# Optimization experiments

Hardware: AMD Instinct MI355X
Metric: run time of the kernel (lower is better)

Reference implementation:

```python
import jax, jax.numpy as jnp
import numpy as np

B, S, H = 2, 2048, 3072
NH, NKV, HD = 24, 8, 128  # num_heads, num_kv_heads, head_dim


def setup_inputs() -> dict:
    key = jax.random.key(0)
    ks = jax.random.split(key, 5)
    scale = 0.02
    return {
        "hidden_states": jax.random.normal(ks[0], (B, S, H), dtype=jnp.float32),
        "attention_mask": jnp.zeros((B, 1, S, S), dtype=jnp.float32),
        "Wq": jax.random.normal(ks[1], (H, NH * HD), dtype=jnp.float32) * scale,
        "Wk": jax.random.normal(ks[2], (H, NKV * HD), dtype=jnp.float32) * scale,
        "Wv": jax.random.normal(ks[3], (H, NKV * HD), dtype=jnp.float32) * scale,
        "Wo": jax.random.normal(ks[4], (NH * HD, H), dtype=jnp.float32) * scale,
    }


def reference(hidden_states, attention_mask, Wq, Wk, Wv, Wo):
    b, s, _ = hidden_states.shape
    n_rep = NH // NKV
    # projections
    q = (hidden_states @ Wq).reshape(b, s, NH, HD).transpose(0, 2, 1, 3)   # [B,NH,S,D]
    k = (hidden_states @ Wk).reshape(b, s, NKV, HD).transpose(0, 2, 1, 3)  # [B,NKV,S,D]
    v = (hidden_states @ Wv).reshape(b, s, NKV, HD).transpose(0, 2, 1, 3)
    # grouped-query attention: view q as [B, NKV, n_rep, S, D]; avoids materializing repeated KV
    qg = q.reshape(b, NKV, n_rep, s, HD)
    scores = jnp.einsum("bgrqd,bgkd->bgrqk", qg, k) / jnp.sqrt(jnp.float32(HD))
    scores = scores.reshape(b, NH, s, s) + attention_mask
    attn = jax.nn.softmax(scores.astype(jnp.float32), axis=-1).astype(q.dtype)
    out = jnp.einsum("bgrqk,bgkd->bgrqd", attn.reshape(b, NKV, n_rep, s, s), v)
    out = out.reshape(b, NH, s, HD).transpose(0, 2, 1, 3).reshape(b, s, NH * HD)
    return out @ Wo
```

## Files before the change

### kernel.cpp

```cpp
#include <hip/hip_runtime.h>
#include <hip/hip_bf16.h>
#include <stdint.h>

typedef __attribute__((ext_vector_type(8))) short short8;
typedef __attribute__((ext_vector_type(4))) float f32x4;
typedef __attribute__((ext_vector_type(16))) float f32x16;

#define DEVINL static __device__ __forceinline__

DEVINL unsigned short f2bf(float x) {
  union { float f; unsigned int u; } c; c.f = x;
  unsigned int u = c.u;
  u += 0x7fffu + ((u >> 16) & 1u);
  return (unsigned short)(u >> 16);
}

DEVINL float bf2f(unsigned short x) {
  union { unsigned int u; float f; } c; c.u = ((unsigned int)x) << 16;
  return c.f;
}

DEVINL f32x4 mfma16(short8 a, short8 b, f32x4 c) {
  return __builtin_amdgcn_mfma_f32_16x16x32_bf16(a, b, c, 0, 0, 0);
}

DEVINL f32x16 mfma32(short8 a, short8 b, f32x16 c) {
  return __builtin_amdgcn_mfma_f32_32x32x16_bf16(a, b, c, 0, 0, 0);
}

DEVINL unsigned int cvtpk(float lo, float hi_) {
  unsigned int r;
  asm("v_cvt_pk_bf16_f32 %0, %1, %2" : "=v"(r) : "v"(lo), "v"(hi_));
  return r;
}

DEVINL void pl32swap(unsigned int& a, unsigned int& b) {
  asm("v_permlane32_swap_b32 %0, %1" : "+v"(a), "+v"(b));
}

DEVINL void gload16(const void* g, void* l) {
  __builtin_amdgcn_global_load_lds((const __attribute__((address_space(1))) void*)g,
                                   (__attribute__((address_space(3))) void*)l, 16, 0, 0);
}

static constexpr int BB = 2, SS = 2048, HH = 3072;
static constexpr int NH = 24, NKV = 8, HD = 128, NREP = 3;
static constexpr int MM = BB * SS;
static constexpr int KQ = NH * HD;
static constexpr int KKV = NKV * HD;

__global__ void k_cvt(const float* __restrict__ in, unsigned short* __restrict__ out,
                      int n, float scale) {
  int i = (blockIdx.x * 256 + threadIdx.x) * 4;
  if (i >= n) return;
  float4 v = *reinterpret_cast<const float4*>(in + i);
  ushort4 o;
  o.x = f2bf(v.x * scale); o.y = f2bf(v.y * scale);
  o.z = f2bf(v.z * scale); o.w = f2bf(v.w * scale);
  *reinterpret_cast<ushort4*>(out + i) = o;
}

__global__ void k_tcvt(const float* __restrict__ in, unsigned short* __restrict__ out,
                       int R, int C) {
  __shared__ float t[32][33];
  int tx = threadIdx.x & 31, ty = threadIdx.x >> 5;
  int r0 = blockIdx.y * 32, c0 = blockIdx.x * 32;
#pragma unroll
  for (int i = 0; i < 32; i += 8)
    t[ty + i][tx] = in[(long)(r0 + ty + i) * C + c0 + tx];
  __syncthreads();
#pragma unroll
  for (int i = 0; i < 32; i += 8)
    out[(long)(c0 + ty + i) * R + r0 + tx] = f2bf(t[tx][ty + i]);
}

__global__ void k_vt(const unsigned short* __restrict__ V, unsigned short* __restrict__ VT) {
  __shared__ unsigned short t[32][33];
  int b = blockIdx.z >> 3, kv = blockIdx.z & 7;
  int tx = threadIdx.x & 31, ty = threadIdx.x >> 5;
  int d0 = blockIdx.x * 32, s0 = blockIdx.y * 32;
  const unsigned short* src = V + ((long)b * SS) * KKV + kv * HD;
  unsigned short* dst = VT + (long)(b * NKV + kv) * HD * SS;
#pragma unroll
  for (int i = 0; i < 32; i += 8)
    t[ty + i][tx] = src[(long)(s0 + ty + i) * KKV + d0 + tx];
  __syncthreads();
#pragma unroll
  for (int i = 0; i < 32; i += 8)
    dst[(long)(d0 + ty + i) * SS + s0 + tx] = t[tx][ty + i];
}

template <typename OutT>
__global__ __launch_bounds__(256, 2) void k_gemm(const unsigned short* __restrict__ A,
                                                 const unsigned short* __restrict__ Bt,
                                                 OutT* __restrict__ C,
                                                 int M, int N, int K) {
  __shared__ alignas(16) unsigned short As[128 * 64];
  __shared__ alignas(16) unsigned short Bs[128 * 64];
  const int tid = threadIdx.x;
  const int wave = tid >> 6, lane = tid & 63;
  const int l15 = lane & 15, g = lane >> 4;
  const int wr = wave >> 1, wc = wave & 1;
  const long m0 = (long)blockIdx.y * 128, n0 = (long)blockIdx.x * 128;

  f32x4 acc[4][4] = {{{0.f,0.f,0.f,0.f}}};

  for (long k0 = 0; k0 < K; k0 += 64) {
#pragma unroll
    for (int j = 0; j < 4; ++j) {
      int idx = j * 256 + wave * 64 + lane;
      int row = idx >> 3, sub = idx & 7;
      int sc_ = (sub ^ (row & 7)) * 8;
      gload16(A  + (m0 + row) * K + k0 + sc_, (char*)As + (j * 4 + wave) * 1024);
      gload16(Bt + (n0 + row) * K + k0 + sc_, (char*)Bs + (j * 4 + wave) * 1024);
    }
    __syncthreads();
#pragma unroll
    for (int ks = 0; ks < 2; ++ks) {
      short8 a[4], b[4];
#pragma unroll
      for (int m = 0; m < 4; ++m) {
        int row = wr * 64 + m * 16 + l15;
        int cb = (ks * 64 + g * 16) ^ ((row & 7) << 4);
        a[m] = *reinterpret_cast<const short8*>((const char*)As + row * 128 + cb);
      }
#pragma unroll
      for (int n = 0; n < 4; ++n) {
        int row = wc * 64 + n * 16 + l15;
        int cb = (ks * 64 + g * 16) ^ ((row & 7) << 4);
        b[n] = *reinterpret_cast<const short8*>((const char*)Bs + row * 128 + cb);
      }
#pragma unroll
      for (int m = 0; m < 4; ++m)
#pragma unroll
        for (int n = 0; n < 4; ++n)
          acc[m][n] = mfma16(a[m], b[n], acc[m][n]);
    }
    __syncthreads();
  }

#pragma unroll
  for (int m = 0; m < 4; ++m)
#pragma unroll
    for (int n = 0; n < 4; ++n)
#pragma unroll
      for (int r = 0; r < 4; ++r) {
        long row = m0 + wr * 64 + m * 16 + g * 4 + r;
        long col = n0 + wc * 64 + n * 16 + l15;
        float v = acc[m][n][r];
        if constexpr (sizeof(OutT) == 2) C[row * N + col] = f2bf(v);
        else                             C[row * N + col] = v;
      }
}

__global__ __launch_bounds__(256, 3) void k_attn(const unsigned short* __restrict__ Q,
                                                 const unsigned short* __restrict__ Kb,
                                                 const unsigned short* __restrict__ VT,
                                                 const unsigned short* __restrict__ Mb,
                                                 unsigned short* __restrict__ AO) {
  const int tid = threadIdx.x;
  const int wave = tid >> 6, lane = tid & 63;
  const int l31 = lane & 31, hi = lane >> 5;

  const int bid = blockIdx.x;
  const int id = (bid & 7) * 96 + (bid >> 3);
  const int qt = id & 15;
  const int h  = (id >> 4) % NH;
  const int b  = id / (16 * NH);
  const int kv = h / NREP;
  const int qb = qt * 128 + wave * 32;

  const unsigned short* Qp = Q + ((long)b * SS + qb) * KQ + h * HD;
  const unsigned short* Kp = Kb + (long)b * SS * KKV + kv * HD;
  const unsigned short* Vp = VT + (long)(b * NKV + kv) * HD * SS;
  const unsigned short* Mp = Mb + (long)b * SS * SS + (long)(qb + l31) * SS;

  __shared__ alignas(16) unsigned short Ks[2][64 * 128];
  __shared__ alignas(16) unsigned short Vs[128 * 64];

  const float SC2 = 0.08838834764831845f * 1.4426950408889634f;

  short8 qf[8];
#pragma unroll
  for (int c = 0; c < 8; ++c)
    qf[c] = *reinterpret_cast<const short8*>(Qp + (long)l31 * KQ + c * 16 + hi * 8);

  f32x16 o[4];
#pragma unroll
  for (int dc = 0; dc < 4; ++dc)
#pragma unroll
    for (int r = 0; r < 16; ++r) o[dc][r] = 0.f;
  float mrun = -3e38f, lrun = 0.f;

  auto stageK = [&](int buf, int kt) {
#pragma unroll
    for (int j = 0; j < 4; ++j) {
      int idx = j * 256 + wave * 64 + lane;
      int row = idx >> 4, s = idx & 15;
      int ss = (s & 8) | ((s ^ row) & 7);
      gload16(Kp + (long)(kt + row) * KKV + ss * 8,
              (char*)Ks[buf] + (j * 4 + wave) * 1024);
    }
  };
  auto stageV = [&](int kt) {
#pragma unroll
    for (int j = 0; j < 4; ++j) {
      int idx = j * 256 + wave * 64 + lane;
      int row = idx >> 3, s = idx & 7;
      int ss = s ^ (row & 7);
      gload16(Vp + (long)row * SS + kt + ss * 8,
              (char*)Vs + (j * 4 + wave) * 1024);
    }
  };

  stageK(0, 0);
  __syncthreads();

  for (int t = 0; t < SS / 64; ++t) {
    const int kt = t * 64;
    stageV(kt);
    if (t < SS / 64 - 1) stageK((t + 1) & 1, kt + 64);
    const char* Kt = (const char*)Ks[t & 1];

    f32x16 sc0, sc1;
#pragma unroll
    for (int r = 0; r < 16; ++r) { sc0[r] = 0.f; sc1[r] = 0.f; }
    __builtin_amdgcn_s_setprio(1);
#pragma unroll
    for (int sb = 0; sb < 2; ++sb) {
      const int row = sb * 32 + l31;
#pragma unroll
      for (int ch = 0; ch < 2; ++ch) {
        short8 kf[4];
#pragma unroll
        for (int cc = 0; cc < 4; ++cc) {
          int c = ch * 4 + cc;
          int s = c * 2 + hi;
          int ss = (s & 8) | ((s ^ (row & 7)) & 7);
          kf[cc] = *reinterpret_cast<const short8*>(Kt + row * 256 + ss * 16);
        }
#pragma unroll
        for (int cc = 0; cc < 4; ++cc) {
          if (sb == 0) sc0 = mfma32(kf[cc], qf[ch * 4 + cc], sc0);
          else         sc1 = mfma32(kf[cc], qf[ch * 4 + cc], sc1);
        }
      }
    }
    __builtin_amdgcn_s_setprio(0);

    float tm = -3e38f;
#pragma unroll
    for (int sb = 0; sb < 2; ++sb) {
#pragma unroll
      for (int u = 0; u < 4; ++u) {
        ushort4 mk = *reinterpret_cast<const ushort4*>(Mp + kt + sb * 32 + u * 8 + hi * 4);
#pragma unroll
        for (int e = 0; e < 4; ++e) {
          int r = u * 4 + e;
          float x = (sb ? sc1[r] : sc0[r]) * SC2 + bf2f((&mk.x)[e]);
          if (sb) sc1[r] = x; else sc0[r] = x;
          tm = fmaxf(tm, x);
        }
      }
    }
    tm = fmaxf(tm, __shfl_xor(tm, 32));

    if (!__all(tm <= mrun + 8.f)) {
      float mn = fmaxf(mrun, tm);
      float corr = __builtin_amdgcn_exp2f(mrun - mn);
      mrun = mn;
      lrun *= corr;
#pragma unroll
      for (int r = 0; r < 16; ++r) {
        int qrow = (r & 3) + 8 * (r >> 2) + 4 * hi;
        float cr = __shfl(corr, qrow);
#pragma unroll
        for (int dc = 0; dc < 4; ++dc) o[dc][r] *= cr;
      }
    }

    float ts = 0.f;
#pragma unroll
    for (int r = 0; r < 16; ++r) {
      float p0 = __builtin_amdgcn_exp2f(sc0[r] - mrun);
      float p1 = __builtin_amdgcn_exp2f(sc1[r] - mrun);
      sc0[r] = p0; sc1[r] = p1;
      ts += p0 + p1;
    }
    ts += __shfl_xor(ts, 32);
    lrun += ts;

    __syncthreads();

    __builtin_amdgcn_s_setprio(1);
#pragma unroll
    for (int ks = 0; ks < 4; ++ks) {
      const int R = 8 * (ks & 1);
      unsigned int A0, A1, B0, B1;
      if (ks < 2) {
        A0 = cvtpk(sc0[R + 0], sc0[R + 1]); A1 = cvtpk(sc0[R + 2], sc0[R + 3]);
        B0 = cvtpk(sc0[R + 4], sc0[R + 5]); B1 = cvtpk(sc0[R + 6], sc0[R + 7]);
      } else {
        A0 = cvtpk(sc1[R + 0], sc1[R + 1]); A1 = cvtpk(sc1[R + 2], sc1[R + 3]);
        B0 = cvtpk(sc1[R + 4], sc1[R + 5]); B1 = cvtpk(sc1[R + 6], sc1[R + 7]);
      }
      pl32swap(A0, B0);
      pl32swap(A1, B1);
      union { unsigned int w[4]; short8 v; } pa;
      pa.w[0] = A0; pa.w[1] = A1; pa.w[2] = B0; pa.w[3] = B1;
      short8 vf[4];
#pragma unroll
      for (int dc = 0; dc < 4; ++dc) {
        int row = dc * 32 + l31;
        int ss = (ks * 2 + hi) ^ (row & 7);
        vf[dc] = *reinterpret_cast<const short8*>((const char*)Vs + row * 128 + ss * 16);
      }
#pragma unroll
      for (int dc = 0; dc < 4; ++dc)
        o[dc] = mfma32(pa.v, vf[dc], o[dc]);
    }
    __builtin_amdgcn_s_setprio(0);

    __syncthreads();
  }

  float inv = 1.f / lrun;
#pragma unroll
  for (int r = 0; r < 16; ++r) {
    int qrow = (r & 3) + 8 * (r >> 2) + 4 * hi;
    float ir = __shfl(inv, qrow);
    long row = qb + qrow;
#pragma unroll
    for (int dc = 0; dc < 4; ++dc)
      AO[((long)b * SS + row) * KQ + h * HD + dc * 32 + l31] = f2bf(o[dc][r] * ir);
  }
}

extern "C" void kernel_launch(void* const* d_in, const int* in_sizes, int n_in,
                              void* d_out, int out_size, void* d_ws, size_t ws_size,
                              hipStream_t stream) {
  const float* hidden = (const float*)d_in[0];
  const float* mask   = (const float*)d_in[1];
  const float* Wq     = (const float*)d_in[2];
  const float* Wk     = (const float*)d_in[3];
  const float* Wv     = (const float*)d_in[4];
  const float* Wo     = (const float*)d_in[5];

  char* ws = (char*)d_ws;
  constexpr long SZ_X   = (long)MM * HH * 2;
  constexpr long SZ_WQT = (long)HH * KQ * 2;
  constexpr long SZ_WKT = (long)HH * KKV * 2;
  constexpr long SZ_QKV = (long)MM * KKV * 2;
  unsigned short* Xb  = (unsigned short*)(ws);
  unsigned short* WqT = (unsigned short*)(ws + SZ_X);
  unsigned short* WkT = (unsigned short*)(ws + SZ_X + SZ_WQT);
  unsigned short* WvT = (unsigned short*)(ws + SZ_X + SZ_WQT + SZ_WKT);
  unsigned short* WoT = (unsigned short*)(ws + SZ_X + SZ_WQT + 2 * SZ_WKT);
  unsigned short* Qb  = (unsigned short*)(ws + SZ_X + 2 * SZ_WQT + 2 * SZ_WKT);
  unsigned short* Kb  = (unsigned short*)(ws + 2 * SZ_X + 2 * SZ_WQT + 2 * SZ_WKT);
  unsigned short* Vb  = (unsigned short*)(ws + 2 * SZ_X + 2 * SZ_WQT + 2 * SZ_WKT + SZ_QKV);
  unsigned short* VTb = (unsigned short*)(ws + 2 * SZ_X + 2 * SZ_WQT + 2 * SZ_WKT + 2 * SZ_QKV);
  unsigned short* AOb = (unsigned short*)(ws + 2 * SZ_X + 2 * SZ_WQT + 2 * SZ_WKT + 3 * SZ_QKV);
  unsigned short* Mbf = WqT;

  k_cvt<<<(MM * HH) / 1024, 256, 0, stream>>>(hidden, Xb, MM * HH, 1.0f);
  k_tcvt<<<dim3(KQ / 32, HH / 32), 256, 0, stream>>>(Wq, WqT, HH, KQ);
  k_tcvt<<<dim3(KKV / 32, HH / 32), 256, 0, stream>>>(Wk, WkT, HH, KKV);
  k_tcvt<<<dim3(KKV / 32, HH / 32), 256, 0, stream>>>(Wv, WvT, HH, KKV);
  k_tcvt<<<dim3(KQ / 32, HH / 32), 256, 0, stream>>>(Wo, WoT, KQ, HH);

  k_gemm<unsigned short><<<dim3(KQ / 128, MM / 128), 256, 0, stream>>>(Xb, WqT, Qb, MM, KQ, HH);
  k_gemm<unsigned short><<<dim3(KKV / 128, MM / 128), 256, 0, stream>>>(Xb, WkT, Kb, MM, KKV, HH);
  k_gemm<unsigned short><<<dim3(KKV / 128, MM / 128), 256, 0, stream>>>(Xb, WvT, Vb, MM, KKV, HH);

  k_vt<<<dim3(HD / 32, SS / 32, BB * NKV), 256, 0, stream>>>(Vb, VTb);
  k_cvt<<<(BB * SS * SS) / 1024, 256, 0, stream>>>(mask, Mbf, BB * SS * SS,
                                                   1.4426950408889634f);

  k_attn<<<16 * NH * BB, 256, 0, stream>>>(Qb, Kb, VTb, Mbf, AOb);

  k_gemm<float><<<dim3(HH / 128, MM / 128), 256, 0, stream>>>(AOb, WoT, (float*)d_out, MM, HH, HH);
}
```

Before: 539.4 us.

## Skip zero mask loads in attention, fold softmax scale into Wq, swizzle GEMM blocks

```diff
diff --git a/kernel.cpp b/kernel.cpp
--- a/kernel.cpp
+++ b/kernel.cpp
@@ -60,8 +60,23 @@
   *reinterpret_cast<ushort4*>(out + i) = o;
 }
 
+__global__ void k_zero(int* p) { *p = 0; }
+
+__global__ void k_cvtm(const float* __restrict__ in, unsigned short* __restrict__ out,
+                       int n, float scale, int* __restrict__ flag) {
+  int i = (blockIdx.x * 256 + threadIdx.x) * 4;
+  if (i >= n) return;
+  float4 v = *reinterpret_cast<const float4*>(in + i);
+  ushort4 o;
+  o.x = f2bf(v.x * scale); o.y = f2bf(v.y * scale);
+  o.z = f2bf(v.z * scale); o.w = f2bf(v.w * scale);
+  *reinterpret_cast<ushort4*>(out + i) = o;
+  bool nz = (v.x != 0.f) || (v.y != 0.f) || (v.z != 0.f) || (v.w != 0.f);
+  if (__any(nz) && (threadIdx.x & 63) == 0) atomicOr(flag, 1);
+}
+
 __global__ void k_tcvt(const float* __restrict__ in, unsigned short* __restrict__ out,
-                       int R, int C) {
+                       int R, int C, float scale) {
   __shared__ float t[32][33];
   int tx = threadIdx.x & 31, ty = threadIdx.x >> 5;
   int r0 = blockIdx.y * 32, c0 = blockIdx.x * 32;
@@ -71,7 +86,7 @@
   __syncthreads();
 #pragma unroll
   for (int i = 0; i < 32; i += 8)
-    out[(long)(c0 + ty + i) * R + r0 + tx] = f2bf(t[tx][ty + i]);
+    out[(long)(c0 + ty + i) * R + r0 + tx] = f2bf(t[tx][ty + i] * scale);
 }
 
 __global__ void k_vt(const unsigned short* __restrict__ V, unsigned short* __restrict__ VT) {
@@ -101,7 +116,12 @@
   const int wave = tid >> 6, lane = tid & 63;
   const int l15 = lane & 15, g = lane >> 4;
   const int wr = wave >> 1, wc = wave & 1;
-  const long m0 = (long)blockIdx.y * 128, n0 = (long)blockIdx.x * 128;
+
+  const int gx = gridDim.x;
+  const int flat = blockIdx.y * gx + blockIdx.x;
+  const int cpx = (gx * gridDim.y) >> 3;
+  const int swz = (flat & 7) * cpx + (flat >> 3);
+  const long m0 = (long)(swz / gx) * 128, n0 = (long)(swz % gx) * 128;
 
   f32x4 acc[4][4] = {{{0.f,0.f,0.f,0.f}}};
 
@@ -157,7 +177,8 @@
                                                  const unsigned short* __restrict__ Kb,
                                                  const unsigned short* __restrict__ VT,
                                                  const unsigned short* __restrict__ Mb,
-                                                 unsigned short* __restrict__ AO) {
+                                                 unsigned short* __restrict__ AO,
+                                                 const int* __restrict__ flagp) {
   const int tid = threadIdx.x;
   const int wave = tid >> 6, lane = tid & 63;
   const int l31 = lane & 31, hi = lane >> 5;
@@ -173,12 +194,22 @@
   const unsigned short* Qp = Q + ((long)b * SS + qb) * KQ + h * HD;
   const unsigned short* Kp = Kb + (long)b * SS * KKV + kv * HD;
   const unsigned short* Vp = VT + (long)(b * NKV + kv) * HD * SS;
-  const unsigned short* Mp = Mb + (long)b * SS * SS + (long)(qb + l31) * SS;
-
-  __shared__ alignas(16) unsigned short Ks[2][64 * 128];
+  const unsigned short* Mp = Mb + (long)b * SS * SS + (long)(qb + l31) * SS + hi * 4;
+
+  const int msknz = *flagp;
+
+  __shared__ alignas(16) unsigned short Ks[2 * 64 * 128];
   __shared__ alignas(16) unsigned short Vs[128 * 64];
 
-  const float SC2 = 0.08838834764831845f * 1.4426950408889634f;
+  int koff[8], voff[4];
+#pragma unroll
+  for (int c = 0; c < 8; ++c) {
+    int s = c * 2 + hi;
+    koff[c] = l31 * 256 + (((s & 8) | ((s ^ (l31 & 7)) & 7)) << 4);
+  }
+#pragma unroll
+  for (int ks = 0; ks < 4; ++ks)
+    voff[ks] = l31 * 128 + (((ks * 2 + hi) ^ (l31 & 7)) << 4);
 
   short8 qf[8];
 #pragma unroll
@@ -199,7 +230,7 @@
       int row = idx >> 4, s = idx & 15;
       int ss = (s & 8) | ((s ^ row) & 7);
       gload16(Kp + (long)(kt + row) * KKV + ss * 8,
-              (char*)Ks[buf] + (j * 4 + wave) * 1024);
+              (char*)Ks + buf * 16384 + (j * 4 + wave) * 1024);
     }
   };
   auto stageV = [&](int kt) {
@@ -214,13 +245,23 @@
   };
 
   stageK(0, 0);
-  __syncthreads();
-
-  for (int t = 0; t < SS / 64; ++t) {
+  asm volatile("s_waitcnt vmcnt(0)" ::: "memory");
+  __builtin_amdgcn_s_barrier();
+
+  auto body = [&](int t, int BUF) {
     const int kt = t * 64;
+    const bool last = (t == SS / 64 - 1);
     stageV(kt);
-    if (t < SS / 64 - 1) stageK((t + 1) & 1, kt + 64);
-    const char* Kt = (const char*)Ks[t & 1];
+    if (!last) stageK(BUF ^ 1, kt + 64);
+
+    ushort4 mk[8];
+    if (msknz) {
+#pragma unroll
+      for (int sb = 0; sb < 2; ++sb)
+#pragma unroll
+        for (int u = 0; u < 4; ++u)
+          mk[sb * 4 + u] = *reinterpret_cast<const ushort4*>(Mp + kt + sb * 32 + u * 8);
+    }
 
     f32x16 sc0, sc1;
 #pragma unroll
@@ -228,41 +269,35 @@
     __builtin_amdgcn_s_setprio(1);
 #pragma unroll
     for (int sb = 0; sb < 2; ++sb) {
-      const int row = sb * 32 + l31;
-#pragma unroll
-      for (int ch = 0; ch < 2; ++ch) {
-        short8 kf[4];
-#pragma unroll
-        for (int cc = 0; cc < 4; ++cc) {
-          int c = ch * 4 + cc;
-          int s = c * 2 + hi;
-          int ss = (s & 8) | ((s ^ (row & 7)) & 7);
-          kf[cc] = *reinterpret_cast<const short8*>(Kt + row * 256 + ss * 16);
-        }
-#pragma unroll
-        for (int cc = 0; cc < 4; ++cc) {
-          if (sb == 0) sc0 = mfma32(kf[cc], qf[ch * 4 + cc], sc0);
-          else         sc1 = mfma32(kf[cc], qf[ch * 4 + cc], sc1);
-        }
+      const char* kbp = (const char*)Ks + BUF * 16384 + sb * 8192;
+#pragma unroll
+      for (int c = 0; c < 8; ++c) {
+        short8 kf = *reinterpret_cast<const short8*>(kbp + koff[c]);
+        if (sb == 0) sc0 = mfma32(kf, qf[c], sc0);
+        else         sc1 = mfma32(kf, qf[c], sc1);
       }
     }
     __builtin_amdgcn_s_setprio(0);
 
-    float tm = -3e38f;
-#pragma unroll
-    for (int sb = 0; sb < 2; ++sb) {
-#pragma unroll
-      for (int u = 0; u < 4; ++u) {
-        ushort4 mk = *reinterpret_cast<const ushort4*>(Mp + kt + sb * 32 + u * 8 + hi * 4);
-#pragma unroll
-        for (int e = 0; e < 4; ++e) {
-          int r = u * 4 + e;
-          float x = (sb ? sc1[r] : sc0[r]) * SC2 + bf2f((&mk.x)[e]);
-          if (sb) sc1[r] = x; else sc0[r] = x;
-          tm = fmaxf(tm, x);
-        }
-      }
-    }
+    if (msknz) {
+#pragma unroll
+      for (int sb = 0; sb < 2; ++sb)
+#pragma unroll
+        for (int u = 0; u < 4; ++u)
+#pragma unroll
+          for (int e = 0; e < 4; ++e) {
+            int r = u * 4 + e;
+            if (sb) sc1[r] += bf2f((&mk[sb * 4 + u].x)[e]);
+            else    sc0[r] += bf2f((&mk[sb * 4 + u].x)[e]);
+          }
+    }
+    float ta = -3e38f, tb = -3e38f, tc = -3e38f, td = -3e38f;
+#pragma unroll
+    for (int r = 0; r < 8; ++r) {
+      ta = fmaxf(ta, sc0[r]); tb = fmaxf(tb, sc0[r + 8]);
+      tc = fmaxf(tc, sc1[r]); td = fmaxf(td, sc1[r + 8]);
+    }
+    float tm = fmaxf(fmaxf(ta, tb), fmaxf(tc, td));
     tm = fmaxf(tm, __shfl_xor(tm, 32));
 
     if (!__all(tm <= mrun + 8.f)) {
@@ -279,18 +314,21 @@
       }
     }
 
-    float ts = 0.f;
-#pragma unroll
-    for (int r = 0; r < 16; ++r) {
-      float p0 = __builtin_amdgcn_exp2f(sc0[r] - mrun);
-      float p1 = __builtin_amdgcn_exp2f(sc1[r] - mrun);
-      sc0[r] = p0; sc1[r] = p1;
-      ts += p0 + p1;
-    }
+    float s0a = 0.f, s0b = 0.f, s1a = 0.f, s1b = 0.f;
+#pragma unroll
+    for (int r = 0; r < 8; ++r) {
+      sc0[r]     = __builtin_amdgcn_exp2f(sc0[r] - mrun);     s0a += sc0[r];
+      sc0[r + 8] = __builtin_amdgcn_exp2f(sc0[r + 8] - mrun); s0b += sc0[r + 8];
+      sc1[r]     = __builtin_amdgcn_exp2f(sc1[r] - mrun);     s1a += sc1[r];
+      sc1[r + 8] = __builtin_amdgcn_exp2f(sc1[r + 8] - mrun); s1b += sc1[r + 8];
+    }
+    float ts = (s0a + s0b) + (s1a + s1b);
     ts += __shfl_xor(ts, 32);
     lrun += ts;
 
-    __syncthreads();
+    if (!last) asm volatile("s_waitcnt vmcnt(8)" ::: "memory");
+    else       asm volatile("s_waitcnt vmcnt(0)" ::: "memory");
+    __builtin_amdgcn_s_barrier();
 
     __builtin_amdgcn_s_setprio(1);
 #pragma unroll
@@ -308,21 +346,21 @@
       pl32swap(A1, B1);
       union { unsigned int w[4]; short8 v; } pa;
       pa.w[0] = A0; pa.w[1] = A1; pa.w[2] = B0; pa.w[3] = B1;
-      short8 vf[4];
 #pragma unroll
       for (int dc = 0; dc < 4; ++dc) {
-        int row = dc * 32 + l31;
-        int ss = (ks * 2 + hi) ^ (row & 7);
-        vf[dc] = *reinterpret_cast<const short8*>((const char*)Vs + row * 128 + ss * 16);
-      }
-#pragma unroll
-      for (int dc = 0; dc < 4; ++dc)
-        o[dc] = mfma32(pa.v, vf[dc], o[dc]);
+        short8 vf = *reinterpret_cast<const short8*>((const char*)Vs + dc * 4096 + voff[ks]);
+        o[dc] = mfma32(pa.v, vf, o[dc]);
+      }
     }
     __builtin_amdgcn_s_setprio(0);
 
-    __syncthreads();
-  }
+    if (!last) {
+      asm volatile("s_waitcnt vmcnt(0)" ::: "memory");
+      __builtin_amdgcn_s_barrier();
+    }
+  };
+
+  for (int t = 0; t < SS / 64; t += 2) { body(t, 0); body(t + 1, 1); }
 
   float inv = 1.f / lrun;
 #pragma unroll
@@ -362,22 +400,26 @@
   unsigned short* VTb = (unsigned short*)(ws + 2 * SZ_X + 2 * SZ_WQT + 2 * SZ_WKT + 2 * SZ_QKV);
   unsigned short* AOb = (unsigned short*)(ws + 2 * SZ_X + 2 * SZ_WQT + 2 * SZ_WKT + 3 * SZ_QKV);
   unsigned short* Mbf = WqT;
+  int* flagp = (int*)Vb;
+
+  const float QSCALE = 0.08838834764831845f * 1.4426950408889634f;
 
   k_cvt<<<(MM * HH) / 1024, 256, 0, stream>>>(hidden, Xb, MM * HH, 1.0f);
-  k_tcvt<<<dim3(KQ / 32, HH / 32), 256, 0, stream>>>(Wq, WqT, HH, KQ);
-  k_tcvt<<<dim3(KKV / 32, HH / 32), 256, 0, stream>>>(Wk, WkT, HH, KKV);
-  k_tcvt<<<dim3(KKV / 32, HH / 32), 256, 0, stream>>>(Wv, WvT, HH, KKV);
-  k_tcvt<<<dim3(KQ / 32, HH / 32), 256, 0, stream>>>(Wo, WoT, KQ, HH);
+  k_tcvt<<<dim3(KQ / 32, HH / 32), 256, 0, stream>>>(Wq, WqT, HH, KQ, QSCALE);
+  k_tcvt<<<dim3(KKV / 32, HH / 32), 256, 0, stream>>>(Wk, WkT, HH, KKV, 1.0f);
+  k_tcvt<<<dim3(KKV / 32, HH / 32), 256, 0, stream>>>(Wv, WvT, HH, KKV, 1.0f);
+  k_tcvt<<<dim3(KQ / 32, HH / 32), 256, 0, stream>>>(Wo, WoT, KQ, HH, 1.0f);
 
   k_gemm<unsigned short><<<dim3(KQ / 128, MM / 128), 256, 0, stream>>>(Xb, WqT, Qb, MM, KQ, HH);
   k_gemm<unsigned short><<<dim3(KKV / 128, MM / 128), 256, 0, stream>>>(Xb, WkT, Kb, MM, KKV, HH);
   k_gemm<unsigned short><<<dim3(KKV / 128, MM / 128), 256, 0, stream>>>(Xb, WvT, Vb, MM, KKV, HH);
 
   k_vt<<<dim3(HD / 32, SS / 32, BB * NKV), 256, 0, stream>>>(Vb, VTb);
-  k_cvt<<<(BB * SS * SS) / 1024, 256, 0, stream>>>(mask, Mbf, BB * SS * SS,
-                                                   1.4426950408889634f);
-
-  k_attn<<<16 * NH * BB, 256, 0, stream>>>(Qb, Kb, VTb, Mbf, AOb);
+  k_zero<<<1, 1, 0, stream>>>(flagp);
+  k_cvtm<<<(BB * SS * SS) / 1024, 256, 0, stream>>>(mask, Mbf, BB * SS * SS,
+                                                    1.4426950408889634f, flagp);
+
+  k_attn<<<16 * NH * BB, 256, 0, stream>>>(Qb, Kb, VTb, Mbf, AOb, flagp);
 
   k_gemm<float><<<dim3(HH / 128, MM / 128), 256, 0, stream>>>(AOb, WoT, (float*)d_out, MM, HH, HH);
 }
```

New measurement: 623.2 us. 15.5% more time.
